# Kernel tuning notes

Measured on AMD Instinct MI355X. Metric: run time of the kernel, lower is better.

## Reference

```python
import jax, jax.numpy as jnp
import numpy as np

N, E = 50000, 800000
IN_DIM, HID, OUT_DIM = 128, 96, 64
MAX_REC = 5


def setup_inputs() -> dict:
    key = jax.random.key(0)
    ks = jax.random.split(key, 10)
    g = lambda k, shape, scale: (jax.random.normal(k, shape, jnp.float32) * scale)
    return {
        "x": jax.random.normal(ks[0], (N, IN_DIM), jnp.float32),
        "edge_index": jax.random.randint(ks[1], (2, E), 0, N, jnp.int32),
        "w_in": g(ks[2], (IN_DIM, HID), 0.05),
        "b_in": jnp.zeros((HID,), jnp.float32),
        "tau_w1": g(ks[3], (IN_DIM, 16), 0.08),
        "tau_b1": jnp.zeros((16,), jnp.float32),
        "tau_w2": g(ks[4], (16, 1), 0.25),
        "tau_b2": jnp.zeros((1,), jnp.float32),
        "gru_wih": g(ks[5], (3 * HID, HID), 0.05),
        "gru_whh": g(ks[6], (3 * HID, HID), 0.05),
        "gru_bih": jnp.zeros((3 * HID,), jnp.float32),
        "gru_bhh": jnp.zeros((3 * HID,), jnp.float32),
        "w_out": g(ks[7], (HID, OUT_DIM), 0.05),
        "b_out": jnp.zeros((OUT_DIM,), jnp.float32),
    }


def _gru_cell(inp, h, wih, whh, bih, bhh):
    # torch.nn.GRUCell math; wih/whh are [3H, H] stacked (r, z, n)
    gi = inp @ wih.T + bih  # [N, 3H]
    gh = h @ whh.T + bhh    # [N, 3H]
    ir, iz, inn = jnp.split(gi, 3, axis=-1)
    hr, hz, hn = jnp.split(gh, 3, axis=-1)
    r = jax.nn.sigmoid(ir + hr)
    z = jax.nn.sigmoid(iz + hz)
    n = jnp.tanh(inn + r * hn)
    return (1.0 - z) * n + z * h


def reference(x, edge_index, w_in, b_in, tau_w1, tau_b1, tau_w2, tau_b2,
              gru_wih, gru_whh, gru_bih, gru_bhh, w_out, b_out):
    h = jax.nn.relu(x @ w_in + b_in)  # [N, H]
    tau_val = jax.nn.softplus(jax.nn.relu(x @ tau_w1 + tau_b1) @ tau_w2 + tau_b2)[:, 0]
    # .long() truncates toward zero; tau > 0 so trunc == floor via int cast
    steps = jnp.minimum((1.0 / tau_val).astype(jnp.int32), MAX_REC)  # [N]
    row, col = edge_index[0], edge_index[1]
    for _ in range(MAX_REC):
        d1 = jnp.abs(h[row] - h[col])                       # [E, H]
        agg = jax.ops.segment_sum(d1, row, num_segments=N)  # [N, H]
        new_h = _gru_cell(agg, h, gru_wih, gru_whh, gru_bih, gru_bhh)
        h = jnp.where((steps > 0)[:, None], new_h, h)
        steps = steps - 1
    return h @ w_out + b_out
```

## Files before the change

kernel.cpp:

```cpp
#include <hip/hip_runtime.h>
#include <hip/hip_bf16.h>

#define HID 96
#define INDIM 128
#define OUTDIM 64
#define BM 128
#define GP 128
#define NBF 512

typedef __attribute__((ext_vector_type(8))) _Float16 half8;
typedef __attribute__((ext_vector_type(4))) _Float16 half4;
typedef __attribute__((ext_vector_type(4))) float floatx4;
typedef __attribute__((ext_vector_type(4))) unsigned int uintx4;

__device__ __forceinline__ float ldmix(const void* p, long i, int mode) {
    return mode ? ((const float*)p)[i]
                : __bfloat162float(((const __hip_bfloat16*)p)[i]);
}

__global__ void sniff_kernel(const unsigned int* xw, int* mode) {
    int lane = threadIdx.x & 63;
    int cnt = 0;
    for (int i = lane; i < 4096; i += 64) {
        unsigned int low = xw[i] & 0xFFFFu;
        unsigned int e = (low >> 7) & 0xFFu;
        if (e >= 0xC0u) cnt++;
    }
    #pragma unroll
    for (int ofs = 32; ofs > 0; ofs >>= 1) cnt += __shfl_down(cnt, ofs);
    if (lane == 0) *mode = (cnt > 256) ? 1 : 0;
}

__global__ void prep_kernel(const void* w_in, const void* b_in, const void* tau_w1,
                            const void* tau_b1, const void* tau_w2, const void* tau_b2,
                            const void* wih, const void* whh, const void* bih, const void* bhh,
                            const void* w_out, const void* b_out,
                            _Float16* W2F, _Float16* WinF, _Float16* WoutF,
                            float* tau_w1_f, float* smallf, const int* mode) {
    int m = *mode;
    int tid = blockIdx.x*blockDim.x + threadIdx.x;
    if (tid < 384*192) {
        int c = tid / 192, k = tid % 192;
        int g = c / 96, jj = c % 96;
        float v = 0.f;
        if (k < 96) {
            if (g == 0)      v = ldmix(wih, (long)(jj)*96 + k, m);
            else if (g == 1) v = ldmix(wih, (long)(96+jj)*96 + k, m);
            else if (g == 2) v = ldmix(wih, (long)(192+jj)*96 + k, m);
        } else {
            int kk = k - 96;
            if (g == 0)      v = ldmix(whh, (long)(jj)*96 + kk, m);
            else if (g == 1) v = ldmix(whh, (long)(96+jj)*96 + kk, m);
            else if (g == 3) v = ldmix(whh, (long)(192+jj)*96 + kk, m);
        }
        W2F[tid] = (_Float16)v;
    }
    if (tid < 96*128) {
        int j = tid >> 7, k = tid & 127;
        WinF[tid] = (_Float16)ldmix(w_in, (long)k*96 + j, m);
    }
    if (tid < 64*96) {
        int j = tid / 96, k = tid % 96;
        WoutF[tid] = (_Float16)ldmix(w_out, (long)k*OUTDIM + j, m);
    }
    if (tid < INDIM*16)   tau_w1_f[tid] = ldmix(tau_w1, tid, m);
    if (tid < HID)    smallf[tid]       = ldmix(b_in, tid, m);
    if (tid < 3*HID){ smallf[96+tid]    = ldmix(bih, tid, m);
                      smallf[384+tid]   = ldmix(bhh, tid, m); }
    if (tid < OUTDIM) smallf[672+tid]   = ldmix(b_out, tid, m);
    if (tid < 16)   { smallf[736+tid]   = ldmix(tau_w2, tid, m);
                      smallf[752+tid]   = ldmix(tau_b1, tid, m); }
    if (tid == 0)     smallf[768]       = ldmix(tau_b2, 0, m);
}

__global__ void __launch_bounds__(512) h0_kernel(
        const void* __restrict__ x, const _Float16* __restrict__ WinF,
        const float* __restrict__ smallf, const int* __restrict__ mode,
        _Float16* __restrict__ hN, int N) {
    int row0 = blockIdx.x * BM;
    int jj0 = blockIdx.y * 16;

    __shared__ _Float16 Ah[128*136];
    __shared__ _Float16 Wh[16*136];

    int tid = threadIdx.x;
    int m = *mode;
    long limit = (long)N * INDIM;
    #pragma unroll
    for (int j = 0; j < 8; j++) {
        int e = (tid + j*512) * 4;
        int r = e >> 7, c = e & 127;
        long ge = (long)(row0 + r)*INDIM + c;
        half4 vh = {0, 0, 0, 0};
        if (ge + 4 <= limit) {
            if (m) {
                floatx4 v = *(const floatx4*)((const float*)x + ge);
                #pragma unroll
                for (int q = 0; q < 4; q++) vh[q] = (_Float16)v[q];
            } else {
                const __hip_bfloat16* p = (const __hip_bfloat16*)x + ge;
                #pragma unroll
                for (int q = 0; q < 4; q++) vh[q] = (_Float16)__bfloat162float(p[q]);
            }
        }
        *(half4*)(&Ah[r*136 + c]) = vh;
    }
    if (tid < 256) {
        int wrow = tid >> 4;
        int k = (tid & 15) * 8;
        *(half8*)(&Wh[wrow*136 + k]) = *(const half8*)(WinF + (long)(jj0 + wrow)*INDIM + k);
    }
    __syncthreads();

    int lane = tid & 63;
    int w = tid >> 6;
    int m15 = lane & 15, quad = lane >> 4;
    floatx4 acc = {0.f, 0.f, 0.f, 0.f};
    int abase = (w*16 + m15)*136 + quad*8;
    #pragma unroll
    for (int ks = 0; ks < 4; ks++) {
        int k0 = ks*32;
        half8 a = *(const half8*)(&Ah[abase + k0]);
        half8 b = *(const half8*)(&Wh[m15*136 + quad*8 + k0]);
        acc = __builtin_amdgcn_mfma_f32_16x16x32_f16(a, b, acc, 0, 0, 0);
    }

    int jj = jj0 + m15;
    float b = smallf[jj];
    #pragma unroll
    for (int reg = 0; reg < 4; reg++) {
        int li = row0 + w*16 + quad*4 + reg;
        if (li < N) hN[(long)li*HID + jj] = (_Float16)fmaxf(acc[reg] + b, 0.f);
    }
}

__global__ void __launch_bounds__(256) tau_kernel(
        const void* __restrict__ x, const float* __restrict__ tw,
        const float* __restrict__ smallf, const int* __restrict__ mode,
        int* __restrict__ steps, int N) {
    int n = blockIdx.x*blockDim.x + threadIdx.x;
    int m = *mode;
    int nc = (n < N) ? n : (N - 1);

    float xr[128];
    if (m) {
        const floatx4* xp = (const floatx4*)x + (size_t)nc*32;
        #pragma unroll
        for (int ks = 0; ks < 32; ks++) {
            floatx4 v = xp[ks];
            xr[ks*4+0] = v[0]; xr[ks*4+1] = v[1];
            xr[ks*4+2] = v[2]; xr[ks*4+3] = v[3];
        }
    } else {
        const uintx4* xp = (const uintx4*)((const __hip_bfloat16*)x + (size_t)nc*128);
        #pragma unroll
        for (int ks = 0; ks < 16; ks++) {
            uintx4 v = xp[ks];
            #pragma unroll
            for (int q = 0; q < 4; q++) {
                unsigned int w = v[q];
                xr[ks*8 + q*2 + 0] = __uint_as_float((w & 0xFFFFu) << 16);
                xr[ks*8 + q*2 + 1] = __uint_as_float(w & 0xFFFF0000u);
            }
        }
    }

    float acc[16];
    #pragma unroll
    for (int j = 0; j < 16; j++) acc[j] = 0.f;
    #pragma unroll
    for (int k = 0; k < 128; k++) {
        float xv = xr[k];
        #pragma unroll
        for (int j = 0; j < 16; j++) acc[j] += xv * tw[k*16 + j];
    }

    float z = smallf[768];
    #pragma unroll
    for (int j = 0; j < 16; j++)
        z += fmaxf(acc[j] + smallf[752 + j], 0.f) * smallf[736 + j];
    float tau = fmaxf(z, 0.f) + log1pf(expf(-fabsf(z)));
    float inv = 1.0f / tau;
    int s;
    if (inv >= 5.0f) s = 5;
    else { s = (int)inv; if (s < 0) s = 0; if (s > 5) s = 5; }
    if (n < N) steps[n] = s;
}

__global__ void __launch_bounds__(512) bincnt_kernel(
        const int* __restrict__ row, int E, int NB, int shift, int* __restrict__ bincnt) {
    __shared__ int h[NBF];
    int tid = threadIdx.x;
    int bs = blockDim.x;
    for (int i = tid; i < NB; i += bs) h[i] = 0;
    __syncthreads();
    int stride = gridDim.x * bs;
    for (int e = blockIdx.x*bs + tid; e < E; e += stride)
        atomicAdd(&h[row[e] >> shift], 1);
    __syncthreads();
    for (int i = tid; i < NB; i += bs) {
        int c = h[i];
        if (c) atomicAdd(&bincnt[i], c);
    }
}

__global__ void binscan_kernel(const int* __restrict__ bincnt, int NB, int E, int N,
                               int* __restrict__ bin_start, int* __restrict__ bincur,
                               int* __restrict__ off) {
    __shared__ int vals[NBF];
    __shared__ int part[256];
    int tid = threadIdx.x;
    int per = (NB + 255) / 256;
    int base = tid * per;
    int s = 0;
    for (int j = 0; j < per; j++) {
        int i = base + j;
        int v = (i < NB) ? bincnt[i] : 0;
        if (i < NBF) vals[i] = s;
        s += v;
    }
    part[tid] = s;
    __syncthreads();
    for (int ofs = 1; ofs < 256; ofs <<= 1) {
        int t = (tid >= ofs) ? part[tid - ofs] : 0;
        __syncthreads();
        part[tid] += t;
        __syncthreads();
    }
    int add = (tid == 0) ? 0 : part[tid - 1];
    for (int j = 0; j < per; j++) {
        int i = base + j;
        if (i < NB) {
            int v = vals[i] + add;
            bin_start[i] = v;
            bincur[i] = v;
        }
    }
    if (tid == 0) { bin_start[NB] = E; off[N] = E; }
}

__global__ void __launch_bounds__(512) binfill_kernel(
        const int* __restrict__ row, const int* __restrict__ col,
        int E, int NB, int shift, int* __restrict__ bincur,
        unsigned int* __restrict__ binbuf) {
    __shared__ int h[NBF];
    __shared__ int bs[NBF];
    int tid = threadIdx.x;
    int bsz = blockDim.x;
    int chunk = (E + gridDim.x - 1) / gridDim.x;
    int c0 = blockIdx.x * chunk;
    int c1 = min(c0 + chunk, E);
    for (int i = tid; i < NB; i += bsz) h[i] = 0;
    __syncthreads();
    for (int e = c0 + tid; e < c1; e += bsz)
        atomicAdd(&h[row[e] >> shift], 1);
    __syncthreads();
    for (int i = tid; i < NB; i += bsz) {
        int c = h[i];
        if (c) { bs[i] = atomicAdd(&bincur[i], c); h[i] = 0; }
    }
    __syncthreads();
    unsigned int mask = (1u << shift) - 1u;
    for (int e = c0 + tid; e < c1; e += bsz) {
        int r = row[e];
        int b = r >> shift;
        int p = atomicAdd(&h[b], 1);
        binbuf[bs[b] + p] = ((unsigned int)(r & mask) << 24) | (unsigned int)col[e];
    }
}

__global__ void __launch_bounds__(256) bincsr_kernel(
        const unsigned int* __restrict__ binbuf,
        const int* __restrict__ bin_start, int N, int shift,
        int* __restrict__ off, int* __restrict__ csr_col) {
    __shared__ int hist[256];
    __shared__ int pfx[256];
    int b = blockIdx.x;
    int tid = threadIdx.x;
    int BINSZ = 1 << shift;
    int s0 = bin_start[b], s1 = bin_start[b + 1];
    if (tid < BINSZ) hist[tid] = 0;
    __syncthreads();
    for (int e = s0 + tid; e < s1; e += 256)
        atomicAdd(&hist[binbuf[e] >> 24], 1);
    __syncthreads();
    if (tid == 0) {
        int run = 0;
        for (int j = 0; j < BINSZ; j++) { pfx[j] = run; run += hist[j]; }
    }
    __syncthreads();
    if (tid < BINSZ) {
        int node = (b << shift) + tid;
        if (node < N) off[node] = s0 + pfx[tid];
        hist[tid] = pfx[tid];
    }
    __syncthreads();
    for (int e = s0 + tid; e < s1; e += 256) {
        unsigned int pk = binbuf[e];
        int lr = pk >> 24;
        int p = atomicAdd(&hist[lr], 1);
        csr_col[s0 + p] = (int)(pk & 0xFFFFFFu);
    }
}

__global__ void partial_kernel(const int* __restrict__ steps, int N, int C,
                               int* __restrict__ blksum) {
    __shared__ int red[256*8];
    int tid = threadIdx.x;
    int tg = blockIdx.x*256 + tid;
    int start = tg*C, end = min(start + C, N);
    if (end < start) end = start;
    int cnt[6] = {0,0,0,0,0,0};
    for (int i = start; i < end; i++) cnt[steps[i]]++;
    #pragma unroll
    for (int k = 0; k < 6; k++) red[tid*8 + k] = cnt[k];
    __syncthreads();
    for (int ofs = 128; ofs > 0; ofs >>= 1) {
        if (tid < ofs) {
            #pragma unroll
            for (int k = 0; k < 6; k++) red[tid*8 + k] += red[(tid+ofs)*8 + k];
        }
        __syncthreads();
    }
    if (tid < 6) blksum[blockIdx.x*8 + tid] = red[tid];
}

__global__ void base_kernel(const int* __restrict__ blksum, int* __restrict__ bstart,
                            int* __restrict__ blkbase) {
    __shared__ int tot[8];
    __shared__ int sb[8];
    int tid = threadIdx.x;
    if (tid < 6) {
        int s = 0;
        for (int b = 0; b < GP; b++) s += blksum[b*8 + tid];
        tot[tid] = s;
    }
    __syncthreads();
    if (tid == 0) {
        int run = 0;
        for (int ss = 5; ss >= 0; --ss) { sb[ss] = run; bstart[ss] = run; run += tot[ss]; }
        bstart[6] = run;
    }
    __syncthreads();
    if (tid < 6) {
        int run = sb[tid];
        for (int b = 0; b < GP; b++) { blkbase[b*8 + tid] = run; run += blksum[b*8 + tid]; }
    }
}

__global__ void scatter_kernel(const int* __restrict__ steps, const int* __restrict__ blkbase,
                               int N, int C, int* __restrict__ order) {
    __shared__ int buf[256];
    int tid = threadIdx.x;
    int b = blockIdx.x;
    int tg = b*256 + tid;
    int start = tg*C, end = min(start + C, N);
    if (end < start) end = start;
    int cnt[6] = {0,0,0,0,0,0};
    for (int i = start; i < end; i++) cnt[steps[i]]++;
    int mybase[6];
    #pragma unroll
    for (int k = 0; k < 6; k++) {
        buf[tid] = cnt[k];
        __syncthreads();
        for (int ofs = 1; ofs < 256; ofs <<= 1) {
            int t = (tid >= ofs) ? buf[tid - ofs] : 0;
            __syncthreads();
            buf[tid] += t;
            __syncthreads();
        }
        mybase[k] = blkbase[b*8 + k] + buf[tid] - cnt[k];
        __syncthreads();
    }
    for (int i = start; i < end; i++) order[mybase[steps[i]]++] = i;
}

__global__ void pack_kernel(const _Float16* __restrict__ hN, const int* __restrict__ order,
                            _Float16* __restrict__ hF, int N) {
    int tid = blockIdx.x*blockDim.x + threadIdx.x;
    if (tid >= N*HID) return;
    int li = tid / HID, f = tid % HID;
    int n = order[li];
    hF[tid] = hN[(size_t)n*HID + f];
}

__global__ void agg_kernel(const _Float16* __restrict__ hN, const int* __restrict__ off,
                           const int* __restrict__ csr_col, const int* __restrict__ order,
                           const int* __restrict__ bstart, int t, _Float16* __restrict__ aggF) {
    int K = bstart[t];
    int total = K * 12;
    int stride = gridDim.x * blockDim.x;
    for (int idx = blockIdx.x*blockDim.x + threadIdx.x; idx < total; idx += stride) {
        int li = idx / 12, fg = idx % 12;
        int f = fg * 8;
        int i = order[li];
        half8 hv = *(const half8*)(hN + (size_t)i*HID + f);
        float hvf[8];
        #pragma unroll
        for (int q = 0; q < 8; q++) hvf[q] = (float)hv[q];
        int e0 = off[i], e1 = off[i+1];
        float acc[8];
        #pragma unroll
        for (int q = 0; q < 8; q++) acc[q] = 0.f;
        int e = e0;
        for (; e + 4 <= e1; e += 4) {
            int c0 = csr_col[e],   c1 = csr_col[e+1];
            int c2 = csr_col[e+2], c3 = csr_col[e+3];
            half8 v0 = *(const half8*)(hN + (size_t)c0*HID + f);
            half8 v1 = *(const half8*)(hN + (size_t)c1*HID + f);
            half8 v2 = *(const half8*)(hN + (size_t)c2*HID + f);
            half8 v3 = *(const half8*)(hN + (size_t)c3*HID + f);
            #pragma unroll
            for (int q = 0; q < 8; q++) {
                acc[q] += fabsf(hvf[q] - (float)v0[q]) + fabsf(hvf[q] - (float)v1[q])
                        + fabsf(hvf[q] - (float)v2[q]) + fabsf(hvf[q] - (float)v3[q]);
            }
        }
        for (; e < e1; e++) {
            int c = csr_col[e];
            half8 v = *(const half8*)(hN + (size_t)c*HID + f);
            #pragma unroll
            for (int q = 0; q < 8; q++) acc[q] += fabsf(hvf[q] - (float)v[q]);
        }
        half8 outv;
        #pragma unroll
        for (int q = 0; q < 8; q++) outv[q] = (_Float16)acc[q];
        *(half8*)(aggF + (size_t)li*HID + f) = outv;
    }
}

__global__ void __launch_bounds__(512) gru_kernel(
        const _Float16* __restrict__ aggF, const _Float16* __restrict__ hFin,
        const _Float16* __restrict__ W2F,
        const float* __restrict__ smallf, const int* __restrict__ bstart, int t,
        const int* __restrict__ order, _Float16* __restrict__ hN,
        _Float16* __restrict__ hFout, int N) {
    int K = bstart[t];
    int row0 = blockIdx.x * BM;
    if (row0 >= K) return;
    int jj0 = blockIdx.y * 16;

    __shared__ _Float16 Ah[128*200];
    __shared__ _Float16 Wh[64*200];

    int tid = threadIdx.x;
    long limit = (long)N * HID;
    #pragma unroll
    for (int j = 0; j < 3; j++) {
        int e = (tid + j*512) * 8;
        {
            int r = e / 96, c = e % 96;
            long ge = (long)(row0 + r)*96 + c;
            half8 va = {0,0,0,0,0,0,0,0}, vh = va;
            if (ge + 8 <= limit) {
                va = *(const half8*)(aggF + ge);
                vh = *(const half8*)(hFin + ge);
            }
            *(half8*)(&Ah[r*200 + c])      = va;
            *(half8*)(&Ah[r*200 + 96 + c]) = vh;
        }
        {
            int wrow = e / 192, k = e % 192;
            int g = wrow >> 4, cc = wrow & 15;
            *(half8*)(&Wh[wrow*200 + k]) = *(const half8*)(W2F + (long)(g*96 + jj0 + cc)*192 + k);
        }
    }
    __syncthreads();

    int lane = tid & 63;
    int w = tid >> 6;
    int m15 = lane & 15, quad = lane >> 4;
    floatx4 acc[4];
    #pragma unroll
    for (int g = 0; g < 4; g++) acc[g] = (floatx4){0.f, 0.f, 0.f, 0.f};

    int abase = (w*16 + m15)*200 + quad*8;
    #pragma unroll
    for (int ks = 0; ks < 6; ks++) {
        int k0 = ks*32;
        half8 a = *(const half8*)(&Ah[abase + k0]);
        #pragma unroll
        for (int g = 0; g < 4; g++) {
            half8 b = *(const half8*)(&Wh[(g*16 + m15)*200 + quad*8 + k0]);
            acc[g] = __builtin_amdgcn_mfma_f32_16x16x32_f16(a, b, acc[g], 0, 0, 0);
        }
    }

    int jj = jj0 + m15;
    float bir = smallf[96+jj],  biz = smallf[192+jj], bin = smallf[288+jj];
    float bhr = smallf[384+jj], bhz = smallf[480+jj], bhn = smallf[576+jj];
    #pragma unroll
    for (int reg = 0; reg < 4; reg++) {
        int li = row0 + w*16 + quad*4 + reg;
        if (li < K) {
            float rp = acc[0][reg] + bir + bhr;
            float zp = acc[1][reg] + biz + bhz;
            float ip = acc[2][reg] + bin;
            float hn = acc[3][reg] + bhn;
            float r  = 1.f/(1.f + expf(-rp));
            float z  = 1.f/(1.f + expf(-zp));
            float nn = tanhf(ip + r*hn);
            int tr = w*16 + quad*4 + reg;
            float hold = (float)Ah[tr*200 + 96 + jj];
            _Float16 v16 = (_Float16)((1.f - z)*nn + z*hold);
            int node = order[li];
            hN[(long)node*HID + jj] = v16;
            hFout[(long)li*HID + jj] = v16;
        }
    }
}

__global__ void __launch_bounds__(512) out_kernel(
        const _Float16* __restrict__ hN, const _Float16* __restrict__ WoutF,
        const float* __restrict__ smallf, void* out, const int* mode, int N) {
    int row0 = blockIdx.x * BM;
    int jj0 = blockIdx.y * 16;

    __shared__ _Float16 Ah[128*104];
    __shared__ _Float16 Wh[16*104];

    int tid = threadIdx.x;
    long limit = (long)N * HID;
    #pragma unroll
    for (int j = 0; j < 3; j++) {
        int e = (tid + j*512) * 8;
        int r = e / 96, c = e % 96;
        long ge = (long)(row0 + r)*HID + c;
        half8 v = {0,0,0,0,0,0,0,0};
        if (ge + 8 <= limit) v = *(const half8*)(hN + ge);
        *(half8*)(&Ah[r*104 + c]) = v;
    }
    if (tid < 192) {
        int wrow = tid / 12;
        int k = (tid % 12) * 8;
        *(half8*)(&Wh[wrow*104 + k]) = *(const half8*)(WoutF + (long)(jj0 + wrow)*HID + k);
    }
    __syncthreads();

    int lane = tid & 63;
    int w = tid >> 6;
    int m15 = lane & 15, quad = lane >> 4;
    floatx4 acc = {0.f, 0.f, 0.f, 0.f};
    int abase = (w*16 + m15)*104 + quad*8;
    #pragma unroll
    for (int ks = 0; ks < 3; ks++) {
        int k0 = ks*32;
        half8 a = *(const half8*)(&Ah[abase + k0]);
        half8 b = *(const half8*)(&Wh[m15*104 + quad*8 + k0]);
        acc = __builtin_amdgcn_mfma_f32_16x16x32_f16(a, b, acc, 0, 0, 0);
    }

    int jj = jj0 + m15;
    float b = smallf[672+jj];
    int m = *mode;
    #pragma unroll
    for (int reg = 0; reg < 4; reg++) {
        int li = row0 + w*16 + quad*4 + reg;
        if (li < N) {
            float v = acc[reg] + b;
            long oi = (long)li*OUTDIM + jj;
            if (m) ((float*)out)[oi] = v;
            else   ((__hip_bfloat16*)out)[oi] = __float2bfloat16(v);
        }
    }
}

extern "C" void kernel_launch(void* const* d_in, const int* in_sizes, int n_in,
                              void* d_out, int out_size, void* d_ws, size_t ws_size,
                              hipStream_t stream) {
    const void* x      = d_in[0];
    const int*  ei     = (const int*)d_in[1];
    const void* w_in   = d_in[2],  *b_in   = d_in[3];
    const void* tau_w1 = d_in[4],  *tau_b1 = d_in[5];
    const void* tau_w2 = d_in[6],  *tau_b2 = d_in[7];
    const void* wih    = d_in[8],  *whh    = d_in[9];
    const void* bih    = d_in[10], *bhh    = d_in[11];
    const void* w_out  = d_in[12], *b_out  = d_in[13];

    int N = in_sizes[0] / INDIM;
    int E = in_sizes[1] / 2;
    const int* row = ei;
    const int* col = ei + E;

    int shift = 7;
    while ((((N + (1 << shift) - 1) >> shift)) > NBF && shift < 8) shift++;
    int NB = (N + (1 << shift) - 1) >> shift;

    char* ws = (char*)d_ws;
    size_t o = 0;
    auto take = [&](size_t bytes) -> char* {
        char* p = ws + o;
        o = (o + bytes + 255) & ~(size_t)255;
        return p;
    };
    _Float16* hN    = (_Float16*)take((size_t)N*HID*2);
    _Float16* hFa   = (_Float16*)take((size_t)N*HID*2);
    _Float16* hFb   = (_Float16*)take((size_t)N*HID*2);
    _Float16* aggF  = (_Float16*)take((size_t)N*HID*2);
    _Float16* W2F   = (_Float16*)take((size_t)384*192*2);
    _Float16* WinF  = (_Float16*)take((size_t)96*128*2);
    _Float16* WoutF = (_Float16*)take((size_t)64*96*2);
    float* tau_w1_f = (float*)take((size_t)INDIM*16*4);
    float* smallf   = (float*)take(1024*4);
    int*   off      = (int*)take((size_t)(N+1)*4);
    int*   csr_col  = (int*)take((size_t)E*4);
    int*   order    = (int*)take((size_t)N*4);
    int*   steps    = (int*)take((size_t)N*4);
    int*   bstart   = (int*)take(64);
    int*   mode     = (int*)take(64);
    int*   blksum   = (int*)take((size_t)GP*8*4);
    int*   blkbase  = (int*)take((size_t)GP*8*4);
    unsigned int* binbuf = (unsigned int*)take((size_t)E*4);
    int*   bin_start = (int*)take((size_t)(NBF+1)*4);
    int*   bincur    = (int*)take((size_t)NBF*4);
    char*  zbase    = ws + o;
    int*   bincnt   = (int*)take((size_t)NBF*4);
    size_t zbytes   = (size_t)((ws + o) - zbase);

    hipMemsetAsync(zbase, 0, zbytes, stream);
    sniff_kernel<<<1, 64, 0, stream>>>((const unsigned int*)x, mode);

    prep_kernel<<<(384*192 + 255)/256, 256, 0, stream>>>(
        w_in, b_in, tau_w1, tau_b1, tau_w2, tau_b2, wih, whh, bih, bhh, w_out, b_out,
        W2F, WinF, WoutF, tau_w1_f, smallf, mode);

    dim3 hgrid((N + BM - 1)/BM, 6);
    h0_kernel<<<hgrid, 512, 0, stream>>>(x, WinF, smallf, mode, hN, N);
    tau_kernel<<<(N + 255)/256, 256, 0, stream>>>(x, tau_w1_f, smallf, mode, steps, N);

    bincnt_kernel<<<256, 512, 0, stream>>>(row, E, NB, shift, bincnt);
    binscan_kernel<<<1, 256, 0, stream>>>(bincnt, NB, E, N, bin_start, bincur, off);
    binfill_kernel<<<256, 512, 0, stream>>>(row, col, E, NB, shift, bincur, binbuf);
    bincsr_kernel<<<NB, 256, 0, stream>>>(binbuf, bin_start, N, shift, off, csr_col);

    int C = (N + GP*256 - 1) / (GP*256);
    partial_kernel<<<GP, 256, 0, stream>>>(steps, N, C, blksum);
    base_kernel<<<1, 64, 0, stream>>>(blksum, bstart, blkbase);
    scatter_kernel<<<GP, 256, 0, stream>>>(steps, blkbase, N, C, order);

    pack_kernel<<<(N*HID + 255)/256, 256, 0, stream>>>(hN, order, hFa, N);

    dim3 ggrid((N + BM - 1)/BM, 6);
    _Float16* hin = hFa;
    _Float16* hout = hFb;
    for (int t = 0; t < 5; t++) {
        agg_kernel<<<4096, 256, 0, stream>>>(hN, off, csr_col, order, bstart, t, aggF);
        gru_kernel<<<ggrid, 512, 0, stream>>>(aggF, hin, W2F, smallf, bstart, t,
                                              order, hN, hout, N);
        _Float16* tmp = hin; hin = hout; hout = tmp;
    }

    dim3 ogrid((N + BM - 1)/BM, 4);
    out_kernel<<<ogrid, 512, 0, stream>>>(hN, WoutF, smallf, d_out, mode, N);
}
```

Before: 348.6 us.

## Compute all output columns per block in GEMM kernels and vectorize pack

The h0, GRU and output kernels drop the column-tile grid dimension. Each block now loads its row tile of activations into shared memory once and loops over every 16-column output tile, instead of having six (or four) blocks each reload the same rows. In the GRU kernel the weight slab for the next column tile is reloaded between iterations, which adds two barriers per tile. Fewer, larger blocks cut redundant global reads of aggF/hFin/x but lower block-level parallelism on a large GPU. The pack kernel also copies half8 vectors instead of single halves.

```diff
diff --git a/kernel.cpp b/kernel.cpp
--- a/kernel.cpp
+++ b/kernel.cpp
@@ -78,10 +78,9 @@
         const float* __restrict__ smallf, const int* __restrict__ mode,
         _Float16* __restrict__ hN, int N) {
     int row0 = blockIdx.x * BM;
-    int jj0 = blockIdx.y * 16;
 
     __shared__ _Float16 Ah[128*136];
-    __shared__ _Float16 Wh[16*136];
+    __shared__ _Float16 Wh[96*136];
 
     int tid = threadIdx.x;
     int m = *mode;
@@ -105,32 +104,39 @@
         }
         *(half4*)(&Ah[r*136 + c]) = vh;
     }
-    if (tid < 256) {
-        int wrow = tid >> 4;
-        int k = (tid & 15) * 8;
-        *(half8*)(&Wh[wrow*136 + k]) = *(const half8*)(WinF + (long)(jj0 + wrow)*INDIM + k);
+    #pragma unroll
+    for (int j = 0; j < 3; j++) {
+        int idx = tid + j*512;
+        int wrow = idx >> 4;
+        int k = (idx & 15) * 8;
+        *(half8*)(&Wh[wrow*136 + k]) = *(const half8*)(WinF + (long)wrow*INDIM + k);
     }
     __syncthreads();
 
     int lane = tid & 63;
     int w = tid >> 6;
     int m15 = lane & 15, quad = lane >> 4;
-    floatx4 acc = {0.f, 0.f, 0.f, 0.f};
     int abase = (w*16 + m15)*136 + quad*8;
-    #pragma unroll
-    for (int ks = 0; ks < 4; ks++) {
-        int k0 = ks*32;
-        half8 a = *(const half8*)(&Ah[abase + k0]);
-        half8 b = *(const half8*)(&Wh[m15*136 + quad*8 + k0]);
-        acc = __builtin_amdgcn_mfma_f32_16x16x32_f16(a, b, acc, 0, 0, 0);
-    }
-
-    int jj = jj0 + m15;
-    float b = smallf[jj];
-    #pragma unroll
-    for (int reg = 0; reg < 4; reg++) {
-        int li = row0 + w*16 + quad*4 + reg;
-        if (li < N) hN[(long)li*HID + jj] = (_Float16)fmaxf(acc[reg] + b, 0.f);
+    half8 a0 = *(const half8*)(&Ah[abase]);
+    half8 a1 = *(const half8*)(&Ah[abase + 32]);
+    half8 a2 = *(const half8*)(&Ah[abase + 64]);
+    half8 a3 = *(const half8*)(&Ah[abase + 96]);
+
+    #pragma unroll
+    for (int jt = 0; jt < 6; jt++) {
+        floatx4 acc = {0.f, 0.f, 0.f, 0.f};
+        int wb = (jt*16 + m15)*136 + quad*8;
+        acc = __builtin_amdgcn_mfma_f32_16x16x32_f16(a0, *(const half8*)(&Wh[wb]),      acc, 0, 0, 0);
+        acc = __builtin_amdgcn_mfma_f32_16x16x32_f16(a1, *(const half8*)(&Wh[wb+32]),   acc, 0, 0, 0);
+        acc = __builtin_amdgcn_mfma_f32_16x16x32_f16(a2, *(const half8*)(&Wh[wb+64]),   acc, 0, 0, 0);
+        acc = __builtin_amdgcn_mfma_f32_16x16x32_f16(a3, *(const half8*)(&Wh[wb+96]),   acc, 0, 0, 0);
+        int jj = jt*16 + m15;
+        float b = smallf[jj];
+        #pragma unroll
+        for (int reg = 0; reg < 4; reg++) {
+            int li = row0 + w*16 + quad*4 + reg;
+            if (li < N) hN[(long)li*HID + jj] = (_Float16)fmaxf(acc[reg] + b, 0.f);
+        }
     }
 }
 
@@ -378,10 +384,10 @@
 __global__ void pack_kernel(const _Float16* __restrict__ hN, const int* __restrict__ order,
                             _Float16* __restrict__ hF, int N) {
     int tid = blockIdx.x*blockDim.x + threadIdx.x;
-    if (tid >= N*HID) return;
-    int li = tid / HID, f = tid % HID;
+    if (tid >= N*12) return;
+    int li = tid / 12, fg = tid % 12;
     int n = order[li];
-    hF[tid] = hN[(size_t)n*HID + f];
+    *(half8*)(hF + (size_t)li*HID + fg*8) = *(const half8*)(hN + (size_t)n*HID + fg*8);
 }
 
 __global__ void agg_kernel(const _Float16* __restrict__ hN, const int* __restrict__ off,
@@ -438,7 +444,6 @@
     int K = bstart[t];
     int row0 = blockIdx.x * BM;
     if (row0 >= K) return;
-    int jj0 = blockIdx.y * 16;
 
     __shared__ _Float16 Ah[128*200];
     __shared__ _Float16 Wh[64*200];
@@ -448,64 +453,84 @@
     #pragma unroll
     for (int j = 0; j < 3; j++) {
         int e = (tid + j*512) * 8;
-        {
-            int r = e / 96, c = e % 96;
-            long ge = (long)(row0 + r)*96 + c;
-            half8 va = {0,0,0,0,0,0,0,0}, vh = va;
-            if (ge + 8 <= limit) {
-                va = *(const half8*)(aggF + ge);
-                vh = *(const half8*)(hFin + ge);
-            }
-            *(half8*)(&Ah[r*200 + c])      = va;
-            *(half8*)(&Ah[r*200 + 96 + c]) = vh;
-        }
-        {
-            int wrow = e / 192, k = e % 192;
-            int g = wrow >> 4, cc = wrow & 15;
-            *(half8*)(&Wh[wrow*200 + k]) = *(const half8*)(W2F + (long)(g*96 + jj0 + cc)*192 + k);
-        }
+        int r = e / 96, c = e % 96;
+        long ge = (long)(row0 + r)*96 + c;
+        half8 va = {0,0,0,0,0,0,0,0}, vh = va;
+        if (ge + 8 <= limit) {
+            va = *(const half8*)(aggF + ge);
+            vh = *(const half8*)(hFin + ge);
+        }
+        *(half8*)(&Ah[r*200 + c])      = va;
+        *(half8*)(&Ah[r*200 + 96 + c]) = vh;
+    }
+    #pragma unroll
+    for (int j = 0; j < 3; j++) {
+        int idx = tid + j*512;
+        int wl = idx / 24;
+        int kk = (idx % 24) * 8;
+        int g = wl >> 4, cc = wl & 15;
+        *(half8*)(&Wh[wl*200 + kk]) = *(const half8*)(W2F + (long)(g*96 + cc)*192 + kk);
     }
     __syncthreads();
 
     int lane = tid & 63;
     int w = tid >> 6;
     int m15 = lane & 15, quad = lane >> 4;
-    floatx4 acc[4];
-    #pragma unroll
-    for (int g = 0; g < 4; g++) acc[g] = (floatx4){0.f, 0.f, 0.f, 0.f};
-
     int abase = (w*16 + m15)*200 + quad*8;
-    #pragma unroll
-    for (int ks = 0; ks < 6; ks++) {
-        int k0 = ks*32;
-        half8 a = *(const half8*)(&Ah[abase + k0]);
-        #pragma unroll
-        for (int g = 0; g < 4; g++) {
-            half8 b = *(const half8*)(&Wh[(g*16 + m15)*200 + quad*8 + k0]);
-            acc[g] = __builtin_amdgcn_mfma_f32_16x16x32_f16(a, b, acc[g], 0, 0, 0);
-        }
-    }
-
-    int jj = jj0 + m15;
-    float bir = smallf[96+jj],  biz = smallf[192+jj], bin = smallf[288+jj];
-    float bhr = smallf[384+jj], bhz = smallf[480+jj], bhn = smallf[576+jj];
-    #pragma unroll
-    for (int reg = 0; reg < 4; reg++) {
-        int li = row0 + w*16 + quad*4 + reg;
-        if (li < K) {
-            float rp = acc[0][reg] + bir + bhr;
-            float zp = acc[1][reg] + biz + bhz;
-            float ip = acc[2][reg] + bin;
-            float hn = acc[3][reg] + bhn;
-            float r  = 1.f/(1.f + expf(-rp));
-            float z  = 1.f/(1.f + expf(-zp));
-            float nn = tanhf(ip + r*hn);
-            int tr = w*16 + quad*4 + reg;
-            float hold = (float)Ah[tr*200 + 96 + jj];
-            _Float16 v16 = (_Float16)((1.f - z)*nn + z*hold);
-            int node = order[li];
-            hN[(long)node*HID + jj] = v16;
-            hFout[(long)li*HID + jj] = v16;
+    half8 a[6];
+    #pragma unroll
+    for (int ks = 0; ks < 6; ks++) a[ks] = *(const half8*)(&Ah[abase + ks*32]);
+
+    #pragma unroll
+    for (int jt = 0; jt < 6; jt++) {
+        floatx4 acc[4];
+        #pragma unroll
+        for (int g = 0; g < 4; g++) acc[g] = (floatx4){0.f, 0.f, 0.f, 0.f};
+        #pragma unroll
+        for (int ks = 0; ks < 6; ks++) {
+            int k0 = ks*32;
+            #pragma unroll
+            for (int g = 0; g < 4; g++) {
+                half8 b = *(const half8*)(&Wh[(g*16 + m15)*200 + quad*8 + k0]);
+                acc[g] = __builtin_amdgcn_mfma_f32_16x16x32_f16(a[ks], b, acc[g], 0, 0, 0);
+            }
+        }
+
+        int jj = jt*16 + m15;
+        float bir = smallf[96+jj],  biz = smallf[192+jj], bin = smallf[288+jj];
+        float bhr = smallf[384+jj], bhz = smallf[480+jj], bhn = smallf[576+jj];
+        #pragma unroll
+        for (int reg = 0; reg < 4; reg++) {
+            int li = row0 + w*16 + quad*4 + reg;
+            if (li < K) {
+                float rp = acc[0][reg] + bir + bhr;
+                float zp = acc[1][reg] + biz + bhz;
+                float ip = acc[2][reg] + bin;
+                float hn = acc[3][reg] + bhn;
+                float r  = 1.f/(1.f + expf(-rp));
+                float z  = 1.f/(1.f + expf(-zp));
+                float nn = tanhf(ip + r*hn);
+                int tr = w*16 + quad*4 + reg;
+                float hold = (float)Ah[tr*200 + 96 + jj];
+                _Float16 v16 = (_Float16)((1.f - z)*nn + z*hold);
+                int node = order[li];
+                hN[(long)node*HID + jj] = v16;
+                hFout[(long)li*HID + jj] = v16;
+            }
+        }
+
+        if (jt < 5) {
+            __syncthreads();
+            #pragma unroll
+            for (int j = 0; j < 3; j++) {
+                int idx = tid + j*512;
+                int wl = idx / 24;
+                int kk = (idx % 24) * 8;
+                int g = wl >> 4, cc = wl & 15;
+                *(half8*)(&Wh[wl*200 + kk]) =
+                    *(const half8*)(W2F + (long)(g*96 + (jt+1)*16 + cc)*192 + kk);
+            }
+            __syncthreads();
         }
     }
 }
@@ -514,10 +539,9 @@
         const _Float16* __restrict__ hN, const _Float16* __restrict__ WoutF,
         const float* __restrict__ smallf, void* out, const int* mode, int N) {
     int row0 = blockIdx.x * BM;
-    int jj0 = blockIdx.y * 16;
 
     __shared__ _Float16 Ah[128*104];
-    __shared__ _Float16 Wh[16*104];
+    __shared__ _Float16 Wh[64*104];
 
     int tid = threadIdx.x;
     long limit = (long)N * HID;
@@ -530,37 +554,44 @@
         if (ge + 8 <= limit) v = *(const half8*)(hN + ge);
         *(half8*)(&Ah[r*104 + c]) = v;
     }
-    if (tid < 192) {
-        int wrow = tid / 12;
-        int k = (tid % 12) * 8;
-        *(half8*)(&Wh[wrow*104 + k]) = *(const half8*)(WoutF + (long)(jj0 + wrow)*HID + k);
+    #pragma unroll
+    for (int j = 0; j < 2; j++) {
+        int idx = tid + j*512;
+        if (idx < 768) {
+            int wrow = idx / 12;
+            int k = (idx % 12) * 8;
+            *(half8*)(&Wh[wrow*104 + k]) = *(const half8*)(WoutF + (long)wrow*HID + k);
+        }
     }
     __syncthreads();
 
     int lane = tid & 63;
     int w = tid >> 6;
     int m15 = lane & 15, quad = lane >> 4;
-    floatx4 acc = {0.f, 0.f, 0.f, 0.f};
     int abase = (w*16 + m15)*104 + quad*8;
-    #pragma unroll
-    for (int ks = 0; ks < 3; ks++) {
-        int k0 = ks*32;
-        half8 a = *(const half8*)(&Ah[abase + k0]);
-        half8 b = *(const half8*)(&Wh[m15*104 + quad*8 + k0]);
-        acc = __builtin_amdgcn_mfma_f32_16x16x32_f16(a, b, acc, 0, 0, 0);
-    }
-
-    int jj = jj0 + m15;
-    float b = smallf[672+jj];
+    half8 a0 = *(const half8*)(&Ah[abase]);
+    half8 a1 = *(const half8*)(&Ah[abase + 32]);
+    half8 a2 = *(const half8*)(&Ah[abase + 64]);
     int m = *mode;
-    #pragma unroll
-    for (int reg = 0; reg < 4; reg++) {
-        int li = row0 + w*16 + quad*4 + reg;
-        if (li < N) {
-            float v = acc[reg] + b;
-            long oi = (long)li*OUTDIM + jj;
-            if (m) ((float*)out)[oi] = v;
-            else   ((__hip_bfloat16*)out)[oi] = __float2bfloat16(v);
+
+    #pragma unroll
+    for (int jt = 0; jt < 4; jt++) {
+        floatx4 acc = {0.f, 0.f, 0.f, 0.f};
+        int wb = (jt*16 + m15)*104 + quad*8;
+        acc = __builtin_amdgcn_mfma_f32_16x16x32_f16(a0, *(const half8*)(&Wh[wb]),    acc, 0, 0, 0);
+        acc = __builtin_amdgcn_mfma_f32_16x16x32_f16(a1, *(const half8*)(&Wh[wb+32]), acc, 0, 0, 0);
+        acc = __builtin_amdgcn_mfma_f32_16x16x32_f16(a2, *(const half8*)(&Wh[wb+64]), acc, 0, 0, 0);
+        int jj = jt*16 + m15;
+        float b = smallf[672+jj];
+        #pragma unroll
+        for (int reg = 0; reg < 4; reg++) {
+            int li = row0 + w*16 + quad*4 + reg;
+            if (li < N) {
+                float v = acc[reg] + b;
+                long oi = (long)li*OUTDIM + jj;
+                if (m) ((float*)out)[oi] = v;
+                else   ((__hip_bfloat16*)out)[oi] = __float2bfloat16(v);
+            }
         }
     }
 }
@@ -624,8 +655,8 @@
         w_in, b_in, tau_w1, tau_b1, tau_w2, tau_b2, wih, whh, bih, bhh, w_out, b_out,
         W2F, WinF, WoutF, tau_w1_f, smallf, mode);
 
-    dim3 hgrid((N + BM - 1)/BM, 6);
-    h0_kernel<<<hgrid, 512, 0, stream>>>(x, WinF, smallf, mode, hN, N);
+    int gx = (N + BM - 1)/BM;
+    h0_kernel<<<gx, 512, 0, stream>>>(x, WinF, smallf, mode, hN, N);
     tau_kernel<<<(N + 255)/256, 256, 0, stream>>>(x, tau_w1_f, smallf, mode, steps, N);
 
     bincnt_kernel<<<256, 512, 0, stream>>>(row, E, NB, shift, bincnt);
@@ -638,18 +669,16 @@
     base_kernel<<<1, 64, 0, stream>>>(blksum, bstart, blkbase);
     scatter_kernel<<<GP, 256, 0, stream>>>(steps, blkbase, N, C, order);
 
-    pack_kernel<<<(N*HID + 255)/256, 256, 0, stream>>>(hN, order, hFa, N);
-
-    dim3 ggrid((N + BM - 1)/BM, 6);
+    pack_kernel<<<(N*12 + 255)/256, 256, 0, stream>>>(hN, order, hFa, N);
+
     _Float16* hin = hFa;
     _Float16* hout = hFb;
     for (int t = 0; t < 5; t++) {
         agg_kernel<<<4096, 256, 0, stream>>>(hN, off, csr_col, order, bstart, t, aggF);
-        gru_kernel<<<ggrid, 512, 0, stream>>>(aggF, hin, W2F, smallf, bstart, t,
-                                              order, hN, hout, N);
+        gru_kernel<<<gx, 512, 0, stream>>>(aggF, hin, W2F, smallf, bstart, t,
+                                           order, hN, hout, N);
         _Float16* tmp = hin; hin = hout; hout = tmp;
     }
 
-    dim3 ogrid((N + BM - 1)/BM, 4);
-    out_kernel<<<ogrid, 512, 0, stream>>>(hN, WoutF, smallf, d_out, mode, N);
-}
+    out_kernel<<<gx, 512, 0, stream>>>(hN, WoutF, smallf, d_out, mode, N);
+}
```

Result: slower. 365.2 us (+4.7%).
